# Performance work log

Hardware: AMD Instinct MI355X
Metric: run time of the kernel (lower is better)

## Reference

```python
import jax, jax.numpy as jnp
import numpy as np

B, S, HID = 2, 2048, 2048
NH, NKV, D = 16, 4, 128
EPS = 1e-6
THETA = 1000000.0
SCALE = D ** -0.5


def _rmsnorm(x, w):
    # per-head RMSNorm over last dim (head_dim)
    var = jnp.mean(x * x, axis=-1, keepdims=True)
    return x * jax.lax.rsqrt(var + EPS) * w


def _rope(pos, x):
    # neox-style rotary over full head_dim. x: [B,S,h,D], pos: [B,S]
    half = D // 2
    inv_freq = THETA ** (-jnp.arange(half, dtype=jnp.float32) / half)  # theta^(-2i/D)
    freqs = pos.astype(jnp.float32)[..., None] * inv_freq              # [B,S,half]
    cos = jnp.cos(freqs)[:, :, None, :]
    sin = jnp.sin(freqs)[:, :, None, :]
    x1, x2 = x[..., :half], x[..., half:]
    return jnp.concatenate([x1 * cos - x2 * sin, x2 * cos + x1 * sin], axis=-1)


def setup_inputs() -> dict:
    key = jax.random.key(0)
    ks = jax.random.split(key, 6)
    hidden_states = jax.random.normal(ks[0], (B, S, HID), dtype=jnp.float32)
    positions = jnp.tile(jnp.arange(S, dtype=jnp.int32)[None, :], (B, 1))
    sd = 0.02
    Wq = jax.random.normal(ks[1], (HID, NH * D), dtype=jnp.float32) * sd
    Wk = jax.random.normal(ks[2], (HID, NKV * D), dtype=jnp.float32) * sd
    Wv = jax.random.normal(ks[3], (HID, NKV * D), dtype=jnp.float32) * sd
    Wo = jax.random.normal(ks[4], (NH * D, HID), dtype=jnp.float32) * sd
    q_norm_w = jnp.ones((D,), dtype=jnp.float32)
    k_norm_w = jnp.ones((D,), dtype=jnp.float32)
    return {"hidden_states": hidden_states, "positions": positions,
            "Wq": Wq, "Wk": Wk, "Wv": Wv, "Wo": Wo,
            "q_norm_w": q_norm_w, "k_norm_w": k_norm_w}


def reference(hidden_states, positions, Wq, Wk, Wv, Wo, q_norm_w, k_norm_w):
    # QKV projections (no bias)
    q = (hidden_states @ Wq).reshape(B, S, NH, D)
    k = (hidden_states @ Wk).reshape(B, S, NKV, D)
    v = (hidden_states @ Wv).reshape(B, S, NKV, D)
    # per-head RMSNorm
    q = _rmsnorm(q, q_norm_w)
    k = _rmsnorm(k, k_norm_w)
    # rotary embedding
    q = _rope(positions, q)
    k = _rope(positions, k)
    # GQA: expand kv heads to q heads
    rep = NH // NKV
    k = jnp.repeat(k, rep, axis=2)  # [B,S,NH,D]
    v = jnp.repeat(v, rep, axis=2)
    # non-causal (ENCODER_ONLY) attention
    scores = jnp.einsum('bqhd,bkhd->bhqk', q, k) * SCALE
    attn = jax.nn.softmax(scores, axis=-1)
    ctx = jnp.einsum('bhqk,bkhd->bqhd', attn, v).reshape(B, S, NH * D)
    out = ctx @ Wo
    return out
```

## Files before the change

### kernel.cpp

```cpp
#include <hip/hip_runtime.h>

typedef unsigned short ushort_t;
typedef __attribute__((ext_vector_type(8))) short short8;
typedef __attribute__((ext_vector_type(4))) ushort_t ushort4_t;
typedef __attribute__((ext_vector_type(4))) float f32x4;

#define Bb 2
#define Ss 2048
#define HID 2048
#define NH 16
#define NKV 4
#define Dd 128
constexpr float EPS_ = 1e-6f;
constexpr float THETA_ = 1000000.0f;
constexpr float SCALE_ = 0.08838834764831845f;
constexpr float C2_ = 0.12753785f;
constexpr float THR_RAW_ = 23.5f;

__device__ __forceinline__ ushort_t f2bf(float x) {
  union { float f; unsigned u; } v; v.f = x;
  unsigned r = (v.u + 0x7fffu + ((v.u >> 16) & 1u)) >> 16;
  return (ushort_t)r;
}
__device__ __forceinline__ float bf2f(ushort_t u) {
  union { unsigned u; float f; } v; v.u = ((unsigned)u) << 16;
  return v.f;
}

typedef const __attribute__((address_space(1))) void* gas1_t;
typedef __attribute__((address_space(3))) void* las3_t;
__device__ __forceinline__ void gload_lds16(const void* g, void* l) {
  __builtin_amdgcn_global_load_lds((gas1_t)g, (las3_t)l, 16, 0, 0);
}

__device__ __forceinline__ void store_out(float* p, float v) { *p = v; }
__device__ __forceinline__ void store_out(ushort_t* p, float v) { *p = f2bf(v); }

__global__ __launch_bounds__(256) void convert_f32_bf16(
    const float* __restrict__ src, ushort_t* __restrict__ dst, long n) {
  long i = ((long)blockIdx.x * 256 + threadIdx.x) * 8;
  if (i + 7 < n) {
    float4 v0 = *(const float4*)(src + i);
    float4 v1 = *(const float4*)(src + i + 4);
    ushort4_t a, b;
    a[0] = f2bf(v0.x); a[1] = f2bf(v0.y); a[2] = f2bf(v0.z); a[3] = f2bf(v0.w);
    b[0] = f2bf(v1.x); b[1] = f2bf(v1.y); b[2] = f2bf(v1.z); b[3] = f2bf(v1.w);
    *(ushort4_t*)(dst + i) = a;
    *(ushort4_t*)(dst + i + 4) = b;
  }
}

__global__ __launch_bounds__(256) void transpose_weights(
    const float* __restrict__ Wq, const float* __restrict__ Wk,
    const float* __restrict__ Wv, const float* __restrict__ Wo,
    ushort_t* __restrict__ WqkvT, ushort_t* __restrict__ WoT) {
  __shared__ float tile[32][33];
  unsigned id = blockIdx.x;
  const float* src;
  ushort_t* dst;
  int C, tX;
  if (id < 4096u) {
    src = Wq; dst = WqkvT; C = 2048; tX = 64;
  } else if (id < 5120u) {
    id -= 4096u; src = Wk; dst = WqkvT + (long)2048 * 2048; C = 512; tX = 16;
  } else if (id < 6144u) {
    id -= 5120u; src = Wv; dst = WqkvT + (long)2560 * 2048; C = 512; tX = 16;
  } else {
    id -= 6144u; src = Wo; dst = WoT; C = 2048; tX = 64;
  }
  const int R = 2048;
  int c0 = (id % tX) * 32, r0 = (id / tX) * 32;
  int tx = threadIdx.x & 31, ty = threadIdx.x >> 5;
#pragma unroll
  for (int j = 0; j < 4; j++)
    tile[ty + j * 8][tx] = src[(long)(r0 + ty + j * 8) * C + c0 + tx];
  __syncthreads();
#pragma unroll
  for (int j = 0; j < 4; j++)
    dst[(long)(c0 + ty + j * 8) * R + r0 + tx] = f2bf(tile[tx][ty + j * 8]);
}

template <typename OutT>
__global__ __launch_bounds__(256) void gemm_bt(
    const ushort_t* __restrict__ A, const ushort_t* __restrict__ Bt,
    OutT* __restrict__ C, int M, int N, int K) {
  __shared__ __align__(16) ushort_t As[128 * 32];
  __shared__ __align__(16) ushort_t Bs[128 * 32];
  const int t = threadIdx.x;
  const int wave = t >> 6, lane = t & 63;
  const int wr = wave >> 1, wc = wave & 1;
  const int quad = lane >> 4, l16 = lane & 15;

  unsigned gx = gridDim.x;
  unsigned nwg = gx * gridDim.y;
  unsigned lin = blockIdx.y * gx + blockIdx.x;
  if ((nwg & 7u) == 0u) {
    unsigned cpx = nwg >> 3;
    lin = (lin & 7u) * cpx + (lin >> 3);
  }
  const long bm = (long)(lin / gx) * 128;
  const long bn = (long)(lin % gx) * 128;

  f32x4 acc[4][4] = {};

  const int srow = t >> 2, schunk = t & 3;
  const ushort_t* aSrc = A + (bm + srow) * (long)K + schunk * 8;
  const ushort_t* bSrc = Bt + (bn + srow) * (long)K + schunk * 8;
  const int ldsOff = srow * 32 + schunk * 8;

  for (int k0 = 0; k0 < K; k0 += 32) {
    __syncthreads();
    gload_lds16(aSrc + k0, &As[ldsOff]);
    gload_lds16(aSrc + (long)64 * K + k0, &As[ldsOff + 64 * 32]);
    gload_lds16(bSrc + k0, &Bs[ldsOff]);
    gload_lds16(bSrc + (long)64 * K + k0, &Bs[ldsOff + 64 * 32]);
    __syncthreads();
    short8 af[4], bf[4];
#pragma unroll
    for (int i = 0; i < 4; i++) {
      af[i] = *(const short8*)&As[(wr * 64 + i * 16 + l16) * 32 + quad * 8];
      bf[i] = *(const short8*)&Bs[(wc * 64 + i * 16 + l16) * 32 + quad * 8];
    }
#pragma unroll
    for (int i = 0; i < 4; i++)
#pragma unroll
      for (int j = 0; j < 4; j++)
        acc[i][j] = __builtin_amdgcn_mfma_f32_16x16x32_bf16(af[i], bf[j], acc[i][j], 0, 0, 0);
  }
#pragma unroll
  for (int i = 0; i < 4; i++)
#pragma unroll
    for (int j = 0; j < 4; j++)
#pragma unroll
      for (int r = 0; r < 4; r++) {
        long rr = bm + wr * 64 + i * 16 + quad * 4 + r;
        long cc = bn + wc * 64 + j * 16 + l16;
        store_out(&C[rr * N + cc], acc[i][j][r]);
      }
}

template <typename OutT>
__global__ __launch_bounds__(512) void gemm256_bt(
    const ushort_t* __restrict__ A, const ushort_t* __restrict__ Bt,
    OutT* __restrict__ C, int M, int N, int K) {
  __shared__ __align__(16) ushort_t As[2][256 * 64];
  __shared__ __align__(16) ushort_t Bs[2][256 * 64];
  const int t = threadIdx.x;
  const int wave = t >> 6, lane = t & 63;
  const int wm = wave >> 2, wn = wave & 3;
  const int quad = lane >> 4, l16 = lane & 15;

  unsigned gx = gridDim.x;
  unsigned nwg = gx * gridDim.y;
  unsigned lin = blockIdx.y * gx + blockIdx.x;
  if ((nwg & 7u) == 0u) {
    unsigned cpx = nwg >> 3;
    lin = (lin & 7u) * cpx + (lin >> 3);
  }
  const long bm = (long)(lin / gx) * 256;
  const long bn = (long)(lin % gx) * 256;

  auto stageA = [&](int kt, int ih, int bi) {
    const int k0 = kt * 64;
#pragma unroll
    for (int it = 0; it < 2; it++) {
      int ci = t + it * 512;
      int lr = ci >> 3, cl = ci & 7;
      int row = ((lr & 64) << 1) | (ih << 6) | (lr & 63);
      int cg = cl ^ (row & 7);
      gload_lds16(A + (bm + row) * (long)K + k0 + cg * 8, &As[bi][row * 64 + cl * 8]);
    }
  };
  auto stageB = [&](int kt, int jh, int bi) {
    const int k0 = kt * 64;
#pragma unroll
    for (int it = 0; it < 2; it++) {
      int ci = t + it * 512;
      int lr = ci >> 3, cl = ci & 7;
      int row = ((lr & 96) << 1) | (jh << 5) | (lr & 31);
      int cg = cl ^ (row & 7);
      gload_lds16(Bt + (bn + row) * (long)K + k0 + cg * 8, &Bs[bi][row * 64 + cl * 8]);
    }
  };

  f32x4 acc[8][4] = {};
  short8 af[2][4], bf0[2][2], bf1[2][2];

  const int nt = K >> 6;
  stageA(0, 0, 0); stageA(0, 1, 0); stageB(0, 0, 0); stageB(0, 1, 0);
  stageA(1, 0, 1); stageB(1, 0, 1);
  asm volatile("s_waitcnt vmcnt(4)" ::: "memory");
  __builtin_amdgcn_sched_barrier(0);
  __builtin_amdgcn_s_barrier();
  __builtin_amdgcn_sched_barrier(0);

  const int raBase = (wm * 128 + l16) * 64;
  const int rbBase = (wn * 64 + l16) * 64;
  const int sw = l16 & 7;

  for (int ti = 0; ti < nt; ti++) {
    const int cb = ti & 1;
    const ushort_t* as_ = As[cb];
    const ushort_t* bs_ = Bs[cb];

#pragma unroll
    for (int kk = 0; kk < 2; kk++) {
      int ch = ((kk * 4 + quad) ^ sw) * 8;
#pragma unroll
      for (int di = 0; di < 4; di++)
        af[kk][di] = *(const short8*)&as_[raBase + di * 1024 + ch];
#pragma unroll
      for (int dj = 0; dj < 2; dj++)
        bf0[kk][dj] = *(const short8*)&bs_[rbBase + dj * 1024 + ch];
    }
    if (ti + 1 < nt) stageA(ti + 1, 1, cb ^ 1);
    __builtin_amdgcn_sched_barrier(0);
    __builtin_amdgcn_s_barrier();
    __builtin_amdgcn_sched_barrier(0);
    __builtin_amdgcn_s_setprio(1);
#pragma unroll
    for (int di = 0; di < 4; di++)
#pragma unroll
      for (int dj = 0; dj < 2; dj++)
#pragma unroll
        for (int kk = 0; kk < 2; kk++)
          acc[di][dj] = __builtin_amdgcn_mfma_f32_16x16x32_bf16(af[kk][di], bf0[kk][dj], acc[di][dj], 0, 0, 0);
    __builtin_amdgcn_s_setprio(0);
    __builtin_amdgcn_sched_barrier(0);
    __builtin_amdgcn_s_barrier();
    __builtin_amdgcn_sched_barrier(0);

#pragma unroll
    for (int kk = 0; kk < 2; kk++) {
      int ch = ((kk * 4 + quad) ^ sw) * 8;
#pragma unroll
      for (int dj = 0; dj < 2; dj++)
        bf1[kk][dj] = *(const short8*)&bs_[rbBase + (2 + dj) * 1024 + ch];
    }
    if (ti + 1 < nt) stageB(ti + 1, 1, cb ^ 1);
    __builtin_amdgcn_sched_barrier(0);
    __builtin_amdgcn_s_barrier();
    __builtin_amdgcn_sched_barrier(0);
    __builtin_amdgcn_s_setprio(1);
#pragma unroll
    for (int di = 0; di < 4; di++)
#pragma unroll
      for (int dj = 0; dj < 2; dj++)
#pragma unroll
        for (int kk = 0; kk < 2; kk++)
          acc[di][2 + dj] = __builtin_amdgcn_mfma_f32_16x16x32_bf16(af[kk][di], bf1[kk][dj], acc[di][2 + dj], 0, 0, 0);
    __builtin_amdgcn_s_setprio(0);
    __builtin_amdgcn_sched_barrier(0);
    __builtin_amdgcn_s_barrier();
    __builtin_amdgcn_sched_barrier(0);

#pragma unroll
    for (int kk = 0; kk < 2; kk++) {
      int ch = ((kk * 4 + quad) ^ sw) * 8;
#pragma unroll
      for (int di = 0; di < 4; di++)
        af[kk][di] = *(const short8*)&as_[raBase + (4 + di) * 1024 + ch];
    }
    if (ti + 2 < nt) stageA(ti + 2, 0, cb);
    __builtin_amdgcn_sched_barrier(0);
    __builtin_amdgcn_s_barrier();
    __builtin_amdgcn_sched_barrier(0);
    __builtin_amdgcn_s_setprio(1);
#pragma unroll
    for (int di = 0; di < 4; di++)
#pragma unroll
      for (int dj = 0; dj < 2; dj++)
#pragma unroll
        for (int kk = 0; kk < 2; kk++)
          acc[4 + di][dj] = __builtin_amdgcn_mfma_f32_16x16x32_bf16(af[kk][di], bf0[kk][dj], acc[4 + di][dj], 0, 0, 0);
    __builtin_amdgcn_s_setprio(0);
    __builtin_amdgcn_sched_barrier(0);
    __builtin_amdgcn_s_barrier();
    __builtin_amdgcn_sched_barrier(0);

    if (ti + 2 < nt) stageB(ti + 2, 0, cb);
    __builtin_amdgcn_sched_barrier(0);
    __builtin_amdgcn_s_barrier();
    __builtin_amdgcn_sched_barrier(0);
    __builtin_amdgcn_s_setprio(1);
#pragma unroll
    for (int di = 0; di < 4; di++)
#pragma unroll
      for (int dj = 0; dj < 2; dj++)
#pragma unroll
        for (int kk = 0; kk < 2; kk++)
          acc[4 + di][2 + dj] = __builtin_amdgcn_mfma_f32_16x16x32_bf16(af[kk][di], bf1[kk][dj], acc[4 + di][2 + dj], 0, 0, 0);
    __builtin_amdgcn_s_setprio(0);
    if (ti + 2 < nt) {
      asm volatile("s_waitcnt vmcnt(4)" ::: "memory");
    } else if (ti + 1 < nt) {
      asm volatile("s_waitcnt vmcnt(0)" ::: "memory");
    }
    __builtin_amdgcn_sched_barrier(0);
    __builtin_amdgcn_s_barrier();
    __builtin_amdgcn_sched_barrier(0);
  }

#pragma unroll
  for (int i = 0; i < 8; i++)
#pragma unroll
    for (int j = 0; j < 4; j++)
#pragma unroll
      for (int r = 0; r < 4; r++) {
        long rr = bm + wm * 128 + i * 16 + quad * 4 + r;
        long cc = bn + wn * 64 + j * 16 + l16;
        store_out(&C[rr * N + cc], acc[i][j][r]);
      }
}

__global__ __launch_bounds__(256) void rmsnorm_rope_tv(
    ushort_t* __restrict__ qkv, const int* __restrict__ positions,
    const float* __restrict__ qw, const float* __restrict__ kw,
    ushort_t* __restrict__ Vt) {
  __shared__ ushort_t tile[64][65];
  unsigned bx = blockIdx.x;
  if (bx < 20480u) {
    int gw = bx * 4 + (threadIdx.x >> 6);
    int lane = threadIdx.x & 63;
    int bs = gw / 20, h = gw % 20;
    ushort_t* src = qkv + (long)bs * 3072 + h * 128;
    float x0 = bf2f(src[lane]), x1 = bf2f(src[lane + 64]);
    float ss = x0 * x0 + x1 * x1;
#pragma unroll
    for (int off = 32; off; off >>= 1) ss += __shfl_xor(ss, off);
    float r = rsqrtf(ss * (1.0f / 128.0f) + EPS_);
    const float* w = (h < 16) ? qw : kw;
    x0 = x0 * r * w[lane];
    x1 = x1 * r * w[lane + 64];
    float pos = (float)positions[bs];
    float inv_freq = powf(THETA_, -(float)lane * (1.0f / 64.0f));
    float f = pos * inv_freq;
    float sn, cs;
    sincosf(f, &sn, &cs);
    float o0 = x0 * cs - x1 * sn;
    float o1 = x1 * cs + x0 * sn;
    src[lane] = f2bf(o0);
    src[lane + 64] = f2bf(o1);
  } else {
    unsigned id = bx - 20480u;
    int bxo = id & 31, byo = (id >> 5) & 1, bh = id >> 6;
    int s0 = bxo * 64, d0 = byo * 64;
    int b = bh >> 2, hk = bh & 3;
    int tx = threadIdx.x & 63, ty = threadIdx.x >> 6;
#pragma unroll
    for (int j = 0; j < 16; j++) {
      int sl = j * 4 + ty;
      tile[sl][tx] = qkv[(long)(b * Ss + s0 + sl) * 3072 + 2560 + hk * 128 + d0 + tx];
    }
    __syncthreads();
    const long vtbase = (long)bh * Dd * Ss;
#pragma unroll
    for (int j = 0; j < 16; j++) {
      int dl = j * 4 + ty;
      Vt[vtbase + (long)(d0 + dl) * Ss + s0 + tx] = tile[tx][dl];
    }
  }
}

__global__ __launch_bounds__(512) void flash_attn(
    const ushort_t* __restrict__ qkv, const ushort_t* __restrict__ Vt,
    ushort_t* __restrict__ ctx) {
  __shared__ __align__(16) ushort_t Ks[2][64 * 128];
  __shared__ __align__(16) ushort_t Vs[2][128 * 64];
  __shared__ __align__(16) ushort_t Ps[8][16 * 64];
  const int qt = blockIdx.x, h = blockIdx.y, b = blockIdx.z;
  const int hk = h >> 2;
  const int t = threadIdx.x, wave = t >> 6, lane = t & 63;
  const int quad = lane >> 4, l16 = lane & 15;

  const ushort_t* qp = qkv + (long)(b * Ss + qt * 128) * 3072 + h * 128;
  const ushort_t* kp = qkv + (long)(b * Ss) * 3072 + 2048 + hk * 128;
  const ushort_t* vp = Vt + ((long)(b * NKV + hk) * Dd) * Ss;

  auto stage = [&](int kt, int bi) {
    const int k0 = kt * 64;
#pragma unroll
    for (int it = 0; it < 2; it++) {
      int tt = t + it * 512;
      int row = tt >> 4, cl = tt & 15, cg = cl ^ (row & 15);
      gload_lds16(kp + (long)(k0 + row) * 3072 + cg * 8, &Ks[bi][tt * 8]);
    }
#pragma unroll
    for (int it = 0; it < 2; it++) {
      int tt = t + it * 512;
      int row = tt >> 3, cl = tt & 7, cg = cl ^ (row & 7);
      gload_lds16(vp + (long)row * Ss + k0 + cg * 8, &Vs[bi][tt * 8]);
    }
  };

  stage(0, 0);

  short8 qf[4];
  {
    const ushort_t* qrow = qp + (long)(wave * 16 + l16) * 3072 + quad * 8;
#pragma unroll
    for (int kc = 0; kc < 4; kc++)
      qf[kc] = *(const short8*)(qrow + kc * 32);
  }

  float m_i = -1e30f;
  float l_acc = 0.f;
  f32x4 o[8] = {};

  asm volatile("s_waitcnt vmcnt(0)" ::: "memory");
  __syncthreads();

  int cur = 0;
  for (int kt = 0; kt < Ss / 64; kt++) {
    if (kt + 1 < Ss / 64) stage(kt + 1, cur ^ 1);

    f32x4 sa[4] = {};
    __builtin_amdgcn_s_setprio(1);
#pragma unroll
    for (int kc = 0; kc < 4; kc++) {
#pragma unroll
      for (int nt = 0; nt < 4; nt++) {
        int brow = nt * 16 + l16;
        short8 kfr = *(const short8*)&Ks[cur][brow * 128 + (((kc * 4 + quad) ^ (brow & 15)) * 8)];
        sa[nt] = __builtin_amdgcn_mfma_f32_16x16x32_bf16(kfr, qf[kc], sa[nt], 0, 0, 0);
      }
    }
    __builtin_amdgcn_s_setprio(0);

    float pmax = sa[0][0];
#pragma unroll
    for (int nt = 0; nt < 4; nt++)
#pragma unroll
      for (int r = 0; r < 4; r++) pmax = fmaxf(pmax, sa[nt][r]);

    bool upd = __any(pmax > m_i + THR_RAW_);
    float alpha = 1.0f;
    if (upd) {
      float mx = fmaxf(pmax, __shfl_xor(pmax, 16));
      mx = fmaxf(mx, __shfl_xor(mx, 32));
      float mnew = fmaxf(m_i, mx);
      alpha = __builtin_amdgcn_exp2f((m_i - mnew) * C2_);
      m_i = mnew;
      l_acc *= alpha;
    }

    float mC2 = m_i * C2_;
    float rs = 0.f;
#pragma unroll
    for (int nt = 0; nt < 4; nt++) {
      int cbase = l16 * 64 + ((nt * 2 + (quad >> 1)) ^ (l16 & 7)) * 8 + (quad & 1) * 4;
#pragma unroll
      for (int r = 0; r < 4; r++) {
        float p = __builtin_amdgcn_exp2f(__builtin_fmaf(sa[nt][r], C2_, -mC2));
        rs += p;
        union { float f; unsigned u; } pv; pv.f = p;
        Ps[wave][cbase + r] = (ushort_t)((pv.u + 0x8000u) >> 16);
      }
    }
    l_acc += rs;

    if (upd) {
      float ar0 = __shfl(alpha, quad * 4 + 0);
      float ar1 = __shfl(alpha, quad * 4 + 1);
      float ar2 = __shfl(alpha, quad * 4 + 2);
      float ar3 = __shfl(alpha, quad * 4 + 3);
#pragma unroll
      for (int dt = 0; dt < 8; dt++) {
        o[dt][0] *= ar0; o[dt][1] *= ar1; o[dt][2] *= ar2; o[dt][3] *= ar3;
      }
    }
    asm volatile("s_waitcnt lgkmcnt(0)" ::: "memory");

    __builtin_amdgcn_s_setprio(1);
#pragma unroll
    for (int kc = 0; kc < 2; kc++) {
      int arow = l16;
      short8 af = *(const short8*)&Ps[wave][arow * 64 + (((kc * 4 + quad) ^ (arow & 7)) * 8)];
#pragma unroll
      for (int dt = 0; dt < 8; dt++) {
        int brow = dt * 16 + l16;
        short8 bfr = *(const short8*)&Vs[cur][brow * 64 + (((kc * 4 + quad) ^ (brow & 7)) * 8)];
        o[dt] = __builtin_amdgcn_mfma_f32_16x16x32_bf16(af, bfr, o[dt], 0, 0, 0);
      }
    }
    __builtin_amdgcn_s_setprio(0);

    asm volatile("s_waitcnt vmcnt(0)" ::: "memory");
    __syncthreads();
    cur ^= 1;
  }

  float lt = l_acc + __shfl_xor(l_acc, 16);
  lt += __shfl_xor(lt, 32);
  float linv = 1.0f / lt;
  float lr0 = __shfl(linv, quad * 4 + 0);
  float lr1 = __shfl(linv, quad * 4 + 1);
  float lr2 = __shfl(linv, quad * 4 + 2);
  float lr3 = __shfl(linv, quad * 4 + 3);
  const long obase = (long)(b * Ss + qt * 128 + wave * 16) * (NH * Dd) + h * Dd;
#pragma unroll
  for (int dt = 0; dt < 8; dt++) {
    int col = dt * 16 + l16;
    ctx[obase + (long)(quad * 4 + 0) * (NH * Dd) + col] = f2bf(o[dt][0] * lr0);
    ctx[obase + (long)(quad * 4 + 1) * (NH * Dd) + col] = f2bf(o[dt][1] * lr1);
    ctx[obase + (long)(quad * 4 + 2) * (NH * Dd) + col] = f2bf(o[dt][2] * lr2);
    ctx[obase + (long)(quad * 4 + 3) * (NH * Dd) + col] = f2bf(o[dt][3] * lr3);
  }
}

extern "C" void kernel_launch(void* const* d_in, const int* in_sizes, int n_in,
                              void* d_out, int out_size, void* d_ws, size_t ws_size,
                              hipStream_t stream) {
  const float* hidden = (const float*)d_in[0];
  const int* positions = (const int*)d_in[1];
  const float* Wq = (const float*)d_in[2];
  const float* Wk = (const float*)d_in[3];
  const float* Wv = (const float*)d_in[4];
  const float* Wo = (const float*)d_in[5];
  const float* qw = (const float*)d_in[6];
  const float* kw = (const float*)d_in[7];
  float* out = (float*)d_out;

  char* ws = (char*)d_ws;
  ushort_t* Xbf = (ushort_t*)(ws);
  ushort_t* WqkvT = (ushort_t*)(ws + (16l << 20));
  ushort_t* WoT = (ushort_t*)(ws + (28l << 20));
  ushort_t* qkvb = (ushort_t*)(ws + (36l << 20));
  ushort_t* Vt = (ushort_t*)(ws + (60l << 20));
  ushort_t* ctx = Xbf;

  const long nX = (long)Bb * Ss * HID;
  convert_f32_bf16<<<(unsigned)(nX / 8 / 256), 256, 0, stream>>>(hidden, Xbf, nX);
  transpose_weights<<<10240, 256, 0, stream>>>(Wq, Wk, Wv, Wo, WqkvT, WoT);

  gemm256_bt<ushort_t><<<dim3(3072 / 256, 4096 / 256), 512, 0, stream>>>(Xbf, WqkvT, qkvb, 4096, 3072, 2048);

  rmsnorm_rope_tv<<<20480 + 512, 256, 0, stream>>>(qkvb, positions, qw, kw, Vt);

  flash_attn<<<dim3(Ss / 128, NH, Bb), 512, 0, stream>>>(qkvb, Vt, ctx);

  gemm_bt<float><<<dim3(2048 / 128, 4096 / 128), 256, 0, stream>>>(ctx, WoT, out, 4096, 2048, 2048);
}
```

Before: 339.4 us.

## Process two 16-row query tiles per wave in flash attention with 256 threads

The flash attention kernel now runs 4 waves per block instead of 8, and each wave handles 32 query rows as two 16-row MFMA tiles. Each K and V fragment read from LDS is reused for two MFMAs, which halves LDS read traffic per unit of compute and lets independent MFMA chains interleave. The cost is roughly double the accumulator and register pressure per wave, plus fewer waves to hide latency, which may lower occupancy.

```diff
diff --git a/kernel.cpp b/kernel.cpp
--- a/kernel.cpp
+++ b/kernel.cpp
@@ -362,7 +362,7 @@
   }
 }
 
-__global__ __launch_bounds__(512) void flash_attn(
+__global__ __launch_bounds__(256) void flash_attn(
     const ushort_t* __restrict__ qkv, const ushort_t* __restrict__ Vt,
     ushort_t* __restrict__ ctx) {
   __shared__ __align__(16) ushort_t Ks[2][64 * 128];
@@ -380,14 +380,14 @@
   auto stage = [&](int kt, int bi) {
     const int k0 = kt * 64;
 #pragma unroll
-    for (int it = 0; it < 2; it++) {
-      int tt = t + it * 512;
+    for (int it = 0; it < 4; it++) {
+      int tt = t + it * 256;
       int row = tt >> 4, cl = tt & 15, cg = cl ^ (row & 15);
       gload_lds16(kp + (long)(k0 + row) * 3072 + cg * 8, &Ks[bi][tt * 8]);
     }
 #pragma unroll
-    for (int it = 0; it < 2; it++) {
-      int tt = t + it * 512;
+    for (int it = 0; it < 4; it++) {
+      int tt = t + it * 256;
       int row = tt >> 3, cl = tt & 7, cg = cl ^ (row & 7);
       gload_lds16(vp + (long)row * Ss + k0 + cg * 8, &Vs[bi][tt * 8]);
     }
@@ -395,26 +395,31 @@
 
   stage(0, 0);
 
-  short8 qf[4];
+  short8 qf0[4], qf1[4];
   {
-    const ushort_t* qrow = qp + (long)(wave * 16 + l16) * 3072 + quad * 8;
-#pragma unroll
-    for (int kc = 0; kc < 4; kc++)
-      qf[kc] = *(const short8*)(qrow + kc * 32);
-  }
-
-  float m_i = -1e30f;
-  float l_acc = 0.f;
-  f32x4 o[8] = {};
+    const ushort_t* qrow0 = qp + (long)(wave * 32 + l16) * 3072 + quad * 8;
+    const ushort_t* qrow1 = qrow0 + (long)16 * 3072;
+#pragma unroll
+    for (int kc = 0; kc < 4; kc++) {
+      qf0[kc] = *(const short8*)(qrow0 + kc * 32);
+      qf1[kc] = *(const short8*)(qrow1 + kc * 32);
+    }
+  }
+
+  float m0 = -1e30f, m1 = -1e30f;
+  float l0 = 0.f, l1 = 0.f;
+  f32x4 o0[8] = {}, o1[8] = {};
 
   asm volatile("s_waitcnt vmcnt(0)" ::: "memory");
   __syncthreads();
+
+  const int ps0 = wave * 2, ps1 = wave * 2 + 1;
 
   int cur = 0;
   for (int kt = 0; kt < Ss / 64; kt++) {
     if (kt + 1 < Ss / 64) stage(kt + 1, cur ^ 1);
 
-    f32x4 sa[4] = {};
+    f32x4 sa0[4] = {}, sa1[4] = {};
     __builtin_amdgcn_s_setprio(1);
 #pragma unroll
     for (int kc = 0; kc < 4; kc++) {
@@ -422,51 +427,92 @@
       for (int nt = 0; nt < 4; nt++) {
         int brow = nt * 16 + l16;
         short8 kfr = *(const short8*)&Ks[cur][brow * 128 + (((kc * 4 + quad) ^ (brow & 15)) * 8)];
-        sa[nt] = __builtin_amdgcn_mfma_f32_16x16x32_bf16(kfr, qf[kc], sa[nt], 0, 0, 0);
+        sa0[nt] = __builtin_amdgcn_mfma_f32_16x16x32_bf16(kfr, qf0[kc], sa0[nt], 0, 0, 0);
+        sa1[nt] = __builtin_amdgcn_mfma_f32_16x16x32_bf16(kfr, qf1[kc], sa1[nt], 0, 0, 0);
       }
     }
     __builtin_amdgcn_s_setprio(0);
 
-    float pmax = sa[0][0];
-#pragma unroll
-    for (int nt = 0; nt < 4; nt++)
-#pragma unroll
-      for (int r = 0; r < 4; r++) pmax = fmaxf(pmax, sa[nt][r]);
-
-    bool upd = __any(pmax > m_i + THR_RAW_);
-    float alpha = 1.0f;
-    if (upd) {
-      float mx = fmaxf(pmax, __shfl_xor(pmax, 16));
-      mx = fmaxf(mx, __shfl_xor(mx, 32));
-      float mnew = fmaxf(m_i, mx);
-      alpha = __builtin_amdgcn_exp2f((m_i - mnew) * C2_);
-      m_i = mnew;
-      l_acc *= alpha;
-    }
-
-    float mC2 = m_i * C2_;
-    float rs = 0.f;
-#pragma unroll
-    for (int nt = 0; nt < 4; nt++) {
-      int cbase = l16 * 64 + ((nt * 2 + (quad >> 1)) ^ (l16 & 7)) * 8 + (quad & 1) * 4;
-#pragma unroll
-      for (int r = 0; r < 4; r++) {
-        float p = __builtin_amdgcn_exp2f(__builtin_fmaf(sa[nt][r], C2_, -mC2));
-        rs += p;
-        union { float f; unsigned u; } pv; pv.f = p;
-        Ps[wave][cbase + r] = (ushort_t)((pv.u + 0x8000u) >> 16);
-      }
-    }
-    l_acc += rs;
-
-    if (upd) {
-      float ar0 = __shfl(alpha, quad * 4 + 0);
-      float ar1 = __shfl(alpha, quad * 4 + 1);
-      float ar2 = __shfl(alpha, quad * 4 + 2);
-      float ar3 = __shfl(alpha, quad * 4 + 3);
-#pragma unroll
-      for (int dt = 0; dt < 8; dt++) {
-        o[dt][0] *= ar0; o[dt][1] *= ar1; o[dt][2] *= ar2; o[dt][3] *= ar3;
+    {
+      float pmax = sa0[0][0];
+#pragma unroll
+      for (int nt = 0; nt < 4; nt++)
+#pragma unroll
+        for (int r = 0; r < 4; r++) pmax = fmaxf(pmax, sa0[nt][r]);
+      bool upd = __any(pmax > m0 + THR_RAW_);
+      float alpha = 1.0f;
+      if (upd) {
+        float mx = fmaxf(pmax, __shfl_xor(pmax, 16));
+        mx = fmaxf(mx, __shfl_xor(mx, 32));
+        float mnew = fmaxf(m0, mx);
+        alpha = __builtin_amdgcn_exp2f((m0 - mnew) * C2_);
+        m0 = mnew;
+        l0 *= alpha;
+      }
+      float mC2 = m0 * C2_;
+      float rs = 0.f;
+#pragma unroll
+      for (int nt = 0; nt < 4; nt++) {
+        int cbase = l16 * 64 + ((nt * 2 + (quad >> 1)) ^ (l16 & 7)) * 8 + (quad & 1) * 4;
+#pragma unroll
+        for (int r = 0; r < 4; r++) {
+          float p = __builtin_amdgcn_exp2f(__builtin_fmaf(sa0[nt][r], C2_, -mC2));
+          rs += p;
+          union { float f; unsigned u; } pv; pv.f = p;
+          Ps[ps0][cbase + r] = (ushort_t)((pv.u + 0x8000u) >> 16);
+        }
+      }
+      l0 += rs;
+      if (upd) {
+        float ar0 = __shfl(alpha, quad * 4 + 0);
+        float ar1 = __shfl(alpha, quad * 4 + 1);
+        float ar2 = __shfl(alpha, quad * 4 + 2);
+        float ar3 = __shfl(alpha, quad * 4 + 3);
+#pragma unroll
+        for (int dt = 0; dt < 8; dt++) {
+          o0[dt][0] *= ar0; o0[dt][1] *= ar1; o0[dt][2] *= ar2; o0[dt][3] *= ar3;
+        }
+      }
+    }
+    {
+      float pmax = sa1[0][0];
+#pragma unroll
+      for (int nt = 0; nt < 4; nt++)
+#pragma unroll
+        for (int r = 0; r < 4; r++) pmax = fmaxf(pmax, sa1[nt][r]);
+      bool upd = __any(pmax > m1 + THR_RAW_);
+      float alpha = 1.0f;
+      if (upd) {
+        float mx = fmaxf(pmax, __shfl_xor(pmax, 16));
+        mx = fmaxf(mx, __shfl_xor(mx, 32));
+        float mnew = fmaxf(m1, mx);
+        alpha = __builtin_amdgcn_exp2f((m1 - mnew) * C2_);
+        m1 = mnew;
+        l1 *= alpha;
+      }
+      float mC2 = m1 * C2_;
+      float rs = 0.f;
+#pragma unroll
+      for (int nt = 0; nt < 4; nt++) {
+        int cbase = l16 * 64 + ((nt * 2 + (quad >> 1)) ^ (l16 & 7)) * 8 + (quad & 1) * 4;
+#pragma unroll
+        for (int r = 0; r < 4; r++) {
+          float p = __builtin_amdgcn_exp2f(__builtin_fmaf(sa1[nt][r], C2_, -mC2));
+          rs += p;
+          union { float f; unsigned u; } pv; pv.f = p;
+          Ps[ps1][cbase + r] = (ushort_t)((pv.u + 0x8000u) >> 16);
+        }
+      }
+      l1 += rs;
+      if (upd) {
+        float ar0 = __shfl(alpha, quad * 4 + 0);
+        float ar1 = __shfl(alpha, quad * 4 + 1);
+        float ar2 = __shfl(alpha, quad * 4 + 2);
+        float ar3 = __shfl(alpha, quad * 4 + 3);
+#pragma unroll
+        for (int dt = 0; dt < 8; dt++) {
+          o1[dt][0] *= ar0; o1[dt][1] *= ar1; o1[dt][2] *= ar2; o1[dt][3] *= ar3;
+        }
       }
     }
     asm volatile("s_waitcnt lgkmcnt(0)" ::: "memory");
@@ -474,13 +520,15 @@
     __builtin_amdgcn_s_setprio(1);
 #pragma unroll
     for (int kc = 0; kc < 2; kc++) {
-      int arow = l16;
-      short8 af = *(const short8*)&Ps[wave][arow * 64 + (((kc * 4 + quad) ^ (arow & 7)) * 8)];
+      int aoff = l16 * 64 + (((kc * 4 + quad) ^ (l16 & 7)) * 8);
+      short8 af0 = *(const short8*)&Ps[ps0][aoff];
+      short8 af1 = *(const short8*)&Ps[ps1][aoff];
 #pragma unroll
       for (int dt = 0; dt < 8; dt++) {
         int brow = dt * 16 + l16;
         short8 bfr = *(const short8*)&Vs[cur][brow * 64 + (((kc * 4 + quad) ^ (brow & 7)) * 8)];
-        o[dt] = __builtin_amdgcn_mfma_f32_16x16x32_bf16(af, bfr, o[dt], 0, 0, 0);
+        o0[dt] = __builtin_amdgcn_mfma_f32_16x16x32_bf16(af0, bfr, o0[dt], 0, 0, 0);
+        o1[dt] = __builtin_amdgcn_mfma_f32_16x16x32_bf16(af1, bfr, o1[dt], 0, 0, 0);
       }
     }
     __builtin_amdgcn_s_setprio(0);
@@ -490,21 +538,42 @@
     cur ^= 1;
   }
 
-  float lt = l_acc + __shfl_xor(l_acc, 16);
-  lt += __shfl_xor(lt, 32);
-  float linv = 1.0f / lt;
-  float lr0 = __shfl(linv, quad * 4 + 0);
-  float lr1 = __shfl(linv, quad * 4 + 1);
-  float lr2 = __shfl(linv, quad * 4 + 2);
-  float lr3 = __shfl(linv, quad * 4 + 3);
-  const long obase = (long)(b * Ss + qt * 128 + wave * 16) * (NH * Dd) + h * Dd;
-#pragma unroll
-  for (int dt = 0; dt < 8; dt++) {
-    int col = dt * 16 + l16;
-    ctx[obase + (long)(quad * 4 + 0) * (NH * Dd) + col] = f2bf(o[dt][0] * lr0);
-    ctx[obase + (long)(quad * 4 + 1) * (NH * Dd) + col] = f2bf(o[dt][1] * lr1);
-    ctx[obase + (long)(quad * 4 + 2) * (NH * Dd) + col] = f2bf(o[dt][2] * lr2);
-    ctx[obase + (long)(quad * 4 + 3) * (NH * Dd) + col] = f2bf(o[dt][3] * lr3);
+  const long ldc = NH * Dd;
+  {
+    float lt = l0 + __shfl_xor(l0, 16);
+    lt += __shfl_xor(lt, 32);
+    float linv = 1.0f / lt;
+    float lr0 = __shfl(linv, quad * 4 + 0);
+    float lr1 = __shfl(linv, quad * 4 + 1);
+    float lr2 = __shfl(linv, quad * 4 + 2);
+    float lr3 = __shfl(linv, quad * 4 + 3);
+    const long obase = (long)(b * Ss + qt * 128 + wave * 32) * ldc + h * Dd;
+#pragma unroll
+    for (int dt = 0; dt < 8; dt++) {
+      int col = dt * 16 + l16;
+      ctx[obase + (long)(quad * 4 + 0) * ldc + col] = f2bf(o0[dt][0] * lr0);
+      ctx[obase + (long)(quad * 4 + 1) * ldc + col] = f2bf(o0[dt][1] * lr1);
+      ctx[obase + (long)(quad * 4 + 2) * ldc + col] = f2bf(o0[dt][2] * lr2);
+      ctx[obase + (long)(quad * 4 + 3) * ldc + col] = f2bf(o0[dt][3] * lr3);
+    }
+  }
+  {
+    float lt = l1 + __shfl_xor(l1, 16);
+    lt += __shfl_xor(lt, 32);
+    float linv = 1.0f / lt;
+    float lr0 = __shfl(linv, quad * 4 + 0);
+    float lr1 = __shfl(linv, quad * 4 + 1);
+    float lr2 = __shfl(linv, quad * 4 + 2);
+    float lr3 = __shfl(linv, quad * 4 + 3);
+    const long obase = (long)(b * Ss + qt * 128 + wave * 32 + 16) * ldc + h * Dd;
+#pragma unroll
+    for (int dt = 0; dt < 8; dt++) {
+      int col = dt * 16 + l16;
+      ctx[obase + (long)(quad * 4 + 0) * ldc + col] = f2bf(o1[dt][0] * lr0);
+      ctx[obase + (long)(quad * 4 + 1) * ldc + col] = f2bf(o1[dt][1] * lr1);
+      ctx[obase + (long)(quad * 4 + 2) * ldc + col] = f2bf(o1[dt][2] * lr2);
+      ctx[obase + (long)(quad * 4 + 3) * ldc + col] = f2bf(o1[dt][3] * lr3);
+    }
   }
 }
 
@@ -537,7 +606,7 @@
 
   rmsnorm_rope_tv<<<20480 + 512, 256, 0, stream>>>(qkvb, positions, qw, kw, Vt);
 
-  flash_attn<<<dim3(Ss / 128, NH, Bb), 512, 0, stream>>>(qkvb, Vt, ctx);
+  flash_attn<<<dim3(Ss / 128, NH, Bb), 256, 0, stream>>>(qkvb, Vt, ctx);
 
   gemm_bt<float><<<dim3(2048 / 128, 4096 / 128), 256, 0, stream>>>(ctx, WoT, out, 4096, 2048, 2048);
 }
```

After: 404.9 us. +19.3%, slower.
